# Optimization experiments

Measured on AMD Instinct MI355X. Metric: run time of the kernel, lower is better.

## Reference

```python
import jax, jax.numpy as jnp
import numpy as np

D = 1024           # input_size
D2 = 2 * D         # hidden width of the three inner linears
OUT = 1024         # output_size
S = 8192           # tokens per example


def setup_inputs() -> dict:
    key = jax.random.key(0)
    ks = jax.random.split(key, 11)
    def lin(k, fan_in, fan_out):
        bound = 1.0 / np.sqrt(fan_in)
        kw, kb = jax.random.split(k)
        W = jax.random.uniform(kw, (fan_in, fan_out), jnp.float32, -bound, bound)
        b = jax.random.uniform(kb, (fan_out,), jnp.float32, -bound, bound)
        return W, b
    W_in, b_in = lin(ks[0], D, D2)      # reading_example_input
    W_out, b_out = lin(ks[1], D, D2)    # reading_example_output
    W_cat, b_cat = lin(ks[2], D2, D2)   # concatenated_layer_map
    W_fin, b_fin = lin(ks[3], D2, OUT)  # final_map
    return {
        "input_embedding": jax.random.normal(ks[4], (1, S, D), jnp.float32),
        "output_embedding": jax.random.normal(ks[5], (1, S, D), jnp.float32),
        "random_augmentation": jax.random.normal(ks[6], (1, S, D), jnp.float32),
        "W_in": W_in, "b_in": b_in,
        "W_out": W_out, "b_out": b_out,
        "W_cat": W_cat, "b_cat": b_cat,
        "W_fin": W_fin, "b_fin": b_fin,
    }


def reference(input_embedding, output_embedding, random_augmentation,
              W_in, b_in, W_out, b_out, W_cat, b_cat, W_fin, b_fin):
    def march(x, y):
        # x, y: [1, S, D]
        iq = jax.nn.softmax(x @ W_in + b_in, axis=-1)[0]    # [S, 2D]
        oq = jax.nn.softmax(y @ W_out + b_out, axis=-1)[0]  # [S, 2D]
        cat = jnp.concatenate((x, y), axis=-1)[0]           # [S, 2D]
        icm = jax.nn.softmax(cat @ W_cat + b_cat, axis=-1)  # [S, 2D]
        iqk = iq.T @ icm                                    # [2D, 2D]
        oqk = oq.T @ icm                                    # [2D, 2D]
        meta = jax.nn.relu(iqk @ oqk.T)                     # [2D, 2D]
        scale = jnp.sqrt(jnp.float32(icm.shape[-1]))
        res = (icm @ meta) / scale                          # [S, 2D]
        return jax.nn.relu(res @ W_fin + b_fin)             # [S, OUT]

    transformation = march(input_embedding, output_embedding)
    random_desc = march(input_embedding, random_augmentation)
    return (transformation, random_desc)
```

## Files before the change

kernel.cpp:

```cpp
#include <hip/hip_runtime.h>

#define S_TOK 8192
#define DIM   1024
#define DIM2  2048
#define OUTN  1024

typedef __bf16 bf16x8 __attribute__((ext_vector_type(8)));
typedef float  f32x4  __attribute__((ext_vector_type(4)));
typedef short  s16x8  __attribute__((ext_vector_type(8)));
typedef unsigned short u16x4 __attribute__((ext_vector_type(4)));

__device__ __forceinline__ unsigned short f2bf(float x) {
  unsigned u = __builtin_bit_cast(unsigned, x);
  u = (u + 0x7FFFu + ((u >> 16) & 1u)) >> 16;
  return (unsigned short)u;
}
__device__ __forceinline__ float bf2f(unsigned short u) {
  return __builtin_bit_cast(float, (unsigned)u << 16);
}

__device__ __forceinline__ void gld_lds16(const void* g, void* l) {
  auto* g1 = reinterpret_cast<__attribute__((address_space(1))) unsigned*>(
      (unsigned long long)g);
  auto* l3 = reinterpret_cast<__attribute__((address_space(3))) unsigned*>(
      (unsigned long long)l);
  __builtin_amdgcn_global_load_lds(g1, l3, 16, 0, 0);
}

__device__ __forceinline__ int lds_off(int idx, int k) {
  int b = (idx << 7) + (k << 1);
  b ^= ((idx ^ (idx >> 3)) & 7) << 4;
  return b;
}

__global__ __launch_bounds__(256) void cvt_f32_bf16(const float* __restrict__ in,
                                                    unsigned short* __restrict__ out, int n4) {
  int i = blockIdx.x * 256 + threadIdx.x;
  if (i >= n4) return;
  float4 v = ((const float4*)in)[i];
  u16x4 o;
  o[0] = f2bf(v.x); o[1] = f2bf(v.y); o[2] = f2bf(v.z); o[3] = f2bf(v.w);
  *(u16x4*)(out + (size_t)i * 4) = o;
}

template <int F32IN>
__global__ __launch_bounds__(256) void transpose_to_bf16(const void* __restrict__ in,
                                                         unsigned short* __restrict__ out,
                                                         int R, int C) {
  __shared__ unsigned short t[64 * 64];
  const int r0 = blockIdx.y << 6, c0 = blockIdx.x << 6;
  const int tid = threadIdx.x;
#pragma unroll
  for (int i = 0; i < 2; ++i) {
    int ch = tid + (i << 8);
    int r = ch >> 3, c8 = (ch & 7) << 3;
    s16x8 w;
    if (F32IN) {
      const float* p = (const float*)in + (size_t)(r0 + r) * C + c0 + c8;
      float4 a = *(const float4*)p, b = *(const float4*)(p + 4);
      w[0] = (short)f2bf(a.x); w[1] = (short)f2bf(a.y);
      w[2] = (short)f2bf(a.z); w[3] = (short)f2bf(a.w);
      w[4] = (short)f2bf(b.x); w[5] = (short)f2bf(b.y);
      w[6] = (short)f2bf(b.z); w[7] = (short)f2bf(b.w);
    } else {
      w = *(const s16x8*)((const unsigned short*)in + (size_t)(r0 + r) * C + c0 + c8);
    }
    int sw = ((r ^ (r >> 3)) & 7) << 3;
    *(s16x8*)&t[(r << 6) + (c8 ^ sw)] = w;
  }
  __syncthreads();
#pragma unroll
  for (int i = 0; i < 2; ++i) {
    int ch = tid + (i << 8);
    int c = ch >> 3, r8 = (ch & 7) << 3;
    s16x8 w;
#pragma unroll
    for (int j = 0; j < 8; ++j) {
      int rr = r8 + j;
      w[j] = (short)t[(rr << 6) + (c ^ (((rr ^ (rr >> 3)) & 7) << 3))];
    }
    *(s16x8*)(out + (size_t)(c0 + c) * R + r0 + r8) = w;
  }
}

struct SmTab { unsigned short* T[6]; };
__global__ __launch_bounds__(512) void softmax_cols(SmTab tab) {
  unsigned short* T = tab.T[blockIdx.y];
  const int tid = threadIdx.x;
  const int colg = tid & 63, seg = tid >> 6;
  const size_t c = ((size_t)blockIdx.x << 6) + colg;
  float m = -1e30f, s = 0.f;
  for (int n = seg; n < DIM2; n += 8) {
    float v = bf2f(T[(size_t)n * S_TOK + c]);
    float mn = fmaxf(m, v);
    s = s * __expf(m - mn) + __expf(v - mn);
    m = mn;
  }
  __shared__ float redm[512], reds[512];
  redm[tid] = m; reds[tid] = s;
  __syncthreads();
  if (seg == 0) {
    float M = m, S = s;
#pragma unroll
    for (int k = 1; k < 8; ++k) {
      float mk = redm[colg + (k << 6)], sk = reds[colg + (k << 6)];
      float mn = fmaxf(M, mk);
      S = S * __expf(M - mn) + sk * __expf(mk - mn);
      M = mn;
    }
    redm[colg] = M; reds[colg] = 1.0f / S;
  }
  __syncthreads();
  m = redm[colg];
  const float inv = reds[colg];
  for (int n = seg; n < DIM2; n += 8) {
    size_t idx = (size_t)n * S_TOK + c;
    T[idx] = f2bf(__expf(bf2f(T[idx]) - m) * inv);
  }
}

struct GPtr {
  const unsigned short* A[3];
  const unsigned short* Arow2[3];
  const unsigned short* B[3];
  const unsigned short* Bk2[3];
  const float* bias[3];
  void* C[3];
};

template <int ASPLIT, int BSPLIT, int BIAS_ROW, int OUT_BF16>
__global__ __launch_bounds__(256, 3) void gemm_nt(GPtr p, int lda, int ldb, int ldc,
                                                  int K, float scale, int do_relu) {
  __shared__ __align__(16) char lds[32768];
  char* As = lds;
  char* Bs = lds + 16384;
  const int z = blockIdx.z;
  const int tid  = threadIdx.x;
  const int lane = tid & 63;
  const int wave = tid >> 6;
  const int wm = (wave >> 1) << 6;
  const int wn = (wave & 1) << 6;
  const int m0 = blockIdx.y << 7;
  const int n0 = blockIdx.x << 7;

  const unsigned short* Au = p.A[z];
  int mb = m0;
  if (ASPLIT && m0 >= 2048) { Au = p.Arow2[z]; mb = m0 - 2048; }
  const unsigned short* B  = p.B[z];
  const unsigned short* B2 = BSPLIT ? p.Bk2[z] : B;
  const float* bias = p.bias[z];
  void* Cv = p.C[z];

  int srow[4], sgk[4];
#pragma unroll
  for (int i = 0; i < 4; ++i) {
    int c = (wave << 8) + (i << 6) + lane;
    int row = c >> 3, kc = c & 7;
    srow[i] = row;
    sgk[i]  = (kc ^ ((row ^ (row >> 3)) & 7)) << 3;
  }

  f32x4 acc[4][4];
#pragma unroll
  for (int i = 0; i < 4; ++i)
#pragma unroll
    for (int j = 0; j < 4; ++j) acc[i][j] = {0.f, 0.f, 0.f, 0.f};

  for (int k0 = 0; k0 < K; k0 += 64) {
    const unsigned short* bsrc = B;
    int kb = k0;
    if (BSPLIT && k0 >= DIM) { bsrc = B2; kb = k0 - DIM; }
#pragma unroll
    for (int i = 0; i < 4; ++i) {
      char* dA = As + (((wave << 2) + i) << 10);
      char* dB = Bs + (((wave << 2) + i) << 10);
      gld_lds16(Au   + (size_t)(mb + srow[i]) * lda + k0 + sgk[i], dA);
      gld_lds16(bsrc + (size_t)(n0 + srow[i]) * ldb + kb + sgk[i], dB);
    }
    __syncthreads();
#pragma unroll
    for (int ks = 0; ks < 2; ++ks) {
      bf16x8 af[4], bfr[4];
      int kk = (ks << 5) + ((lane >> 4) << 3);
#pragma unroll
      for (int t = 0; t < 4; ++t) {
        af[t]  = *(const bf16x8*)(As + lds_off(wm + (t << 4) + (lane & 15), kk));
        bfr[t] = *(const bf16x8*)(Bs + lds_off(wn + (t << 4) + (lane & 15), kk));
      }
#pragma unroll
      for (int mt = 0; mt < 4; ++mt)
#pragma unroll
        for (int nt = 0; nt < 4; ++nt)
          acc[mt][nt] = __builtin_amdgcn_mfma_f32_16x16x32_bf16(af[mt], bfr[nt], acc[mt][nt], 0, 0, 0);
    }
    __syncthreads();
  }

#pragma unroll
  for (int nt = 0; nt < 4; ++nt) {
    int col = n0 + wn + (nt << 4) + (lane & 15);
    float bcol = (!BIAS_ROW && bias) ? bias[col] : 0.0f;
#pragma unroll
    for (int mt = 0; mt < 4; ++mt) {
      f32x4 a = acc[mt][nt];
#pragma unroll
      for (int r = 0; r < 4; ++r) {
        int rowg = m0 + wm + (mt << 4) + ((lane >> 4) << 2) + r;
        float bv = BIAS_ROW ? (bias ? bias[rowg] : 0.0f) : bcol;
        float v = a[r] * scale + bv;
        if (do_relu) v = fmaxf(v, 0.0f);
        if (OUT_BF16) ((unsigned short*)Cv)[(size_t)rowg * ldc + col] = f2bf(v);
        else          ((float*)Cv)[(size_t)rowg * ldc + col] = v;
      }
    }
  }
}

template <int ASPLIT, int BSPLIT, int BIAS_ROW, int OUT_BF16>
__global__ __launch_bounds__(512, 2) void gemm256(GPtr p, int lda, int ldb, int ldc,
                                                  int K, float scale, int do_relu) {
  __shared__ __align__(16) char lds[131072];
  const int z = blockIdx.z;
  const int tid  = threadIdx.x;
  const int lane = tid & 63;
  const int wave = tid >> 6;
  const int wm   = wave >> 2;
  const int wn   = wave & 3;

  const int gx = gridDim.x;
  const int nwg = gx * gridDim.y;
  int id = blockIdx.y * gx + blockIdx.x;
  id = (id & 7) * (nwg >> 3) + (id >> 3);
  const int n0 = (id % gx) << 8;
  const int m0 = (id / gx) << 8;

  const unsigned short* Au = p.A[z];
  int mb = m0;
  if (ASPLIT && m0 >= 2048) { Au = p.Arow2[z]; mb = m0 - 2048; }
  const unsigned short* Bp = p.B[z];
  const float* bias = p.bias[z];
  void* Cv = p.C[z];

  const int NT = K >> 6;

  int srow_[2], skel_[2];
#pragma unroll
  for (int i = 0; i < 2; ++i) {
    int row = (i << 7) + (wave << 4) + (lane >> 2);
    srow_[i] = row;
    skel_[i] = ((lane & 3) ^ ((row >> 1) & 3)) << 3;
  }
  const unsigned short* aB[2];
  const unsigned short* bB[2];
  const unsigned short* b2B[2];
#pragma unroll
  for (int i = 0; i < 2; ++i) {
    aB[i]  = Au + (size_t)(mb + srow_[i]) * lda + skel_[i];
    bB[i]  = Bp + (size_t)(n0 + srow_[i]) * ldb + skel_[i];
    b2B[i] = BSPLIT ? (p.Bk2[z] + (size_t)(n0 + srow_[i]) * ldb + skel_[i] - DIM)
                    : bB[i];
  }

  auto stage_unit = [&](int t, int u) {
    const int k0 = t << 6;
    const int h  = u >> 1;
    char* base = lds + ((t & 1) << 16) + ((u & 1) << 15) + (h << 14) + (wave << 10);
#pragma unroll
    for (int i = 0; i < 2; ++i) {
      const unsigned short* src;
      if (u & 1) src = ((BSPLIT && k0 >= DIM) ? b2B[i] : bB[i]) + k0 + (h << 5);
      else       src = aB[i] + k0 + (h << 5);
      gld_lds16(src, base + (i << 13));
    }
  };

  auto rdA = [&](const char* buf, int h, int mf) -> bf16x8 {
    int row = (wm << 7) + (mf << 4) + (lane & 15);
    int col = (lane >> 4) ^ ((row >> 1) & 3);
    return *(const bf16x8*)(buf + (h << 14) + (row << 6) + (col << 4));
  };
  auto rdB = [&](const char* buf, int h, int nf) -> bf16x8 {
    int row = (wn << 6) + (nf << 4) + (lane & 15);
    int col = (lane >> 4) ^ ((row >> 1) & 3);
    return *(const bf16x8*)(buf + 32768 + (h << 14) + (row << 6) + (col << 4));
  };

  f32x4 acc[8][4];
#pragma unroll
  for (int i = 0; i < 8; ++i)
#pragma unroll
    for (int j = 0; j < 4; ++j) acc[i][j] = {0.f, 0.f, 0.f, 0.f};

  stage_unit(0, 0); stage_unit(0, 1); stage_unit(0, 2); stage_unit(0, 3);

  for (int t = 0; t < NT; ++t) {
    const char* buf = lds + ((t & 1) << 16);
    const bool more = (t + 1 < NT);
    bf16x8 aq[4], bq[4];

    if (more) { stage_unit(t + 1, 0); asm volatile("s_waitcnt vmcnt(6)" ::: "memory"); }
    else      { asm volatile("s_waitcnt vmcnt(4)" ::: "memory"); }
    __builtin_amdgcn_s_barrier();
    __builtin_amdgcn_sched_barrier(0);
#pragma unroll
    for (int nf = 0; nf < 4; ++nf) bq[nf] = rdB(buf, 0, nf);
#pragma unroll
    for (int mf = 0; mf < 4; ++mf) aq[mf] = rdA(buf, 0, mf);
    __builtin_amdgcn_s_setprio(1);
#pragma unroll
    for (int mf = 0; mf < 4; ++mf)
#pragma unroll
      for (int nf = 0; nf < 4; ++nf)
        acc[mf][nf] = __builtin_amdgcn_mfma_f32_16x16x32_bf16(aq[mf], bq[nf], acc[mf][nf], 0, 0, 0);
    __builtin_amdgcn_s_setprio(0);
    __builtin_amdgcn_s_barrier();

#pragma unroll
    for (int mf = 0; mf < 4; ++mf) aq[mf] = rdA(buf, 0, mf + 4);
    if (more) stage_unit(t + 1, 1);
    __builtin_amdgcn_s_setprio(1);
#pragma unroll
    for (int mf = 0; mf < 4; ++mf)
#pragma unroll
      for (int nf = 0; nf < 4; ++nf)
        acc[mf + 4][nf] = __builtin_amdgcn_mfma_f32_16x16x32_bf16(aq[mf], bq[nf], acc[mf + 4][nf], 0, 0, 0);
    __builtin_amdgcn_s_setprio(0);
    __builtin_amdgcn_s_barrier();

    if (more) { stage_unit(t + 1, 2); asm volatile("s_waitcnt vmcnt(6)" ::: "memory"); }
    else      { asm volatile("s_waitcnt vmcnt(0)" ::: "memory"); }
    __builtin_amdgcn_s_barrier();
    __builtin_amdgcn_sched_barrier(0);
#pragma unroll
    for (int nf = 0; nf < 4; ++nf) bq[nf] = rdB(buf, 1, nf);
#pragma unroll
    for (int mf = 0; mf < 4; ++mf) aq[mf] = rdA(buf, 1, mf);
    __builtin_amdgcn_s_setprio(1);
#pragma unroll
    for (int mf = 0; mf < 4; ++mf)
#pragma unroll
      for (int nf = 0; nf < 4; ++nf)
        acc[mf][nf] = __builtin_amdgcn_mfma_f32_16x16x32_bf16(aq[mf], bq[nf], acc[mf][nf], 0, 0, 0);
    __builtin_amdgcn_s_setprio(0);
    __builtin_amdgcn_s_barrier();

#pragma unroll
    for (int mf = 0; mf < 4; ++mf) aq[mf] = rdA(buf, 1, mf + 4);
    if (more) stage_unit(t + 1, 3);
    __builtin_amdgcn_s_setprio(1);
#pragma unroll
    for (int mf = 0; mf < 4; ++mf)
#pragma unroll
      for (int nf = 0; nf < 4; ++nf)
        acc[mf + 4][nf] = __builtin_amdgcn_mfma_f32_16x16x32_bf16(aq[mf], bq[nf], acc[mf + 4][nf], 0, 0, 0);
    __builtin_amdgcn_s_setprio(0);
    __builtin_amdgcn_s_barrier();
  }

#pragma unroll
  for (int nf = 0; nf < 4; ++nf) {
    int col = n0 + (wn << 6) + (nf << 4) + (lane & 15);
    float bcol = (!BIAS_ROW && bias) ? bias[col] : 0.0f;
#pragma unroll
    for (int mf = 0; mf < 8; ++mf) {
      f32x4 a = acc[mf][nf];
#pragma unroll
      for (int r = 0; r < 4; ++r) {
        int rowg = m0 + (wm << 7) + (mf << 4) + ((lane >> 4) << 2) + r;
        float bv = BIAS_ROW ? (bias ? bias[rowg] : 0.0f) : bcol;
        float v = a[r] * scale + bv;
        if (do_relu) v = fmaxf(v, 0.0f);
        if (OUT_BF16) ((unsigned short*)Cv)[(size_t)rowg * ldc + col] = f2bf(v);
        else          ((float*)Cv)[(size_t)rowg * ldc + col] = v;
      }
    }
  }
}

extern "C" void kernel_launch(void* const* d_in, const int* in_sizes, int n_in,
                              void* d_out, int out_size, void* d_ws, size_t ws_size,
                              hipStream_t stream) {
  const float* X   = (const float*)d_in[0];
  const float* Y   = (const float*)d_in[1];
  const float* R   = (const float*)d_in[2];
  const float* Wi  = (const float*)d_in[3];
  const float* bi  = (const float*)d_in[4];
  const float* Wo  = (const float*)d_in[5];
  const float* bo  = (const float*)d_in[6];
  const float* Wc  = (const float*)d_in[7];
  const float* bc  = (const float*)d_in[8];
  const float* Wf  = (const float*)d_in[9];
  const float* bf_ = (const float*)d_in[10];
  float* out = (float*)d_out;

  char* ws = (char*)d_ws;
  size_t off = 0;
  auto alloc = [&](size_t b) { char* p = ws + off; off += (b + 255) & ~(size_t)255; return p; };
  unsigned short* Xb   = (unsigned short*)alloc((size_t)S_TOK * DIM  * 2);
  unsigned short* Yb   = (unsigned short*)alloc((size_t)S_TOK * DIM  * 2);
  unsigned short* Rb   = (unsigned short*)alloc((size_t)S_TOK * DIM  * 2);
  unsigned short* WiT  = (unsigned short*)alloc((size_t)DIM2 * DIM  * 2);
  unsigned short* WoT  = (unsigned short*)alloc((size_t)DIM2 * DIM  * 2);
  unsigned short* WcT  = (unsigned short*)alloc((size_t)DIM2 * DIM2 * 2);
  unsigned short* WfT  = (unsigned short*)alloc((size_t)OUTN * DIM2 * 2);
  unsigned short* iqT  = (unsigned short*)alloc((size_t)DIM2 * S_TOK * 2);
  unsigned short* oqT0 = (unsigned short*)alloc((size_t)DIM2 * S_TOK * 2);
  unsigned short* oqT1 = (unsigned short*)alloc((size_t)DIM2 * S_TOK * 2);
  unsigned short* icmT0= (unsigned short*)alloc((size_t)DIM2 * S_TOK * 2);
  unsigned short* icmT1= (unsigned short*)alloc((size_t)DIM2 * S_TOK * 2);
  unsigned short* iqk0 = Xb;
  unsigned short* oqk0 = Xb + (size_t)DIM2*DIM2;
  unsigned short* iqk1 = Yb;
  unsigned short* oqk1 = Yb + (size_t)DIM2*DIM2;
  unsigned short* meta0= iqT;
  unsigned short* meta1= iqT + (size_t)DIM2*DIM2;
  unsigned short* MWT0 = iqT + (size_t)2*DIM2*DIM2;
  unsigned short* MWT1 = iqT + (size_t)2*DIM2*DIM2 + (size_t)OUTN*DIM2;
  unsigned short* icm0 = oqT0;
  unsigned short* icm1 = oqT1;

  auto cvt = [&](const float* s, unsigned short* d, int n) {
    int n4 = n >> 2;
    cvt_f32_bf16<<<dim3((n4 + 255) / 256), dim3(256), 0, stream>>>(s, d, n4);
  };
  cvt(X, Xb, S_TOK * DIM);
  cvt(Y, Yb, S_TOK * DIM);
  cvt(R, Rb, S_TOK * DIM);
  transpose_to_bf16<1><<<dim3(DIM2 / 64, DIM  / 64), 256, 0, stream>>>(Wi, WiT, DIM,  DIM2);
  transpose_to_bf16<1><<<dim3(DIM2 / 64, DIM  / 64), 256, 0, stream>>>(Wo, WoT, DIM,  DIM2);
  transpose_to_bf16<1><<<dim3(DIM2 / 64, DIM2 / 64), 256, 0, stream>>>(Wc, WcT, DIM2, DIM2);
  transpose_to_bf16<1><<<dim3(OUTN / 64, DIM2 / 64), 256, 0, stream>>>(Wf, WfT, DIM2, OUTN);

  const float rscale = 0.022097086912079608f;

  {
    GPtr g{};
    g.A[0] = WiT; g.A[1] = WoT; g.A[2] = WoT;
    g.B[0] = Xb;  g.B[1] = Yb;  g.B[2] = Rb;
    g.bias[0] = bi; g.bias[1] = bo; g.bias[2] = bo;
    g.C[0] = iqT; g.C[1] = oqT0; g.C[2] = oqT1;
    gemm256<0,0,1,1><<<dim3(S_TOK/256, DIM2/256, 3), 512, 0, stream>>>(
        g, DIM, DIM, S_TOK, DIM, 1.f, 0);
  }
  {
    GPtr g{};
    g.A[0] = WcT; g.A[1] = WcT;
    g.B[0] = Xb;  g.B[1] = Xb;
    g.Bk2[0] = Yb; g.Bk2[1] = Rb;
    g.bias[0] = bc; g.bias[1] = bc;
    g.C[0] = icmT0; g.C[1] = icmT1;
    gemm256<0,1,1,1><<<dim3(S_TOK/256, DIM2/256, 2), 512, 0, stream>>>(
        g, DIM2, DIM, S_TOK, DIM2, 1.f, 0);
  }
  {
    SmTab st{};
    st.T[0] = iqT; st.T[1] = oqT0; st.T[2] = oqT1; st.T[3] = icmT0; st.T[4] = icmT1;
    softmax_cols<<<dim3(S_TOK / 64, 5), dim3(512), 0, stream>>>(st);
  }
  {
    GPtr g{};
    g.A[0] = iqT; g.A[1] = iqT;
    g.Arow2[0] = oqT0; g.Arow2[1] = oqT1;
    g.B[0] = icmT0; g.B[1] = icmT1;
    g.C[0] = iqk0; g.C[1] = iqk1;
    gemm256<1,0,0,1><<<dim3(DIM2/256, 4096/256, 2), 512, 0, stream>>>(
        g, S_TOK, S_TOK, DIM2, S_TOK, 1.f, 0);
  }
  transpose_to_bf16<0><<<dim3(S_TOK / 64, DIM2 / 64), 256, 0, stream>>>(icmT0, icm0, DIM2, S_TOK);
  transpose_to_bf16<0><<<dim3(S_TOK / 64, DIM2 / 64), 256, 0, stream>>>(icmT1, icm1, DIM2, S_TOK);
  {
    GPtr g{};
    g.A[0] = iqk0; g.A[1] = iqk1;
    g.B[0] = oqk0; g.B[1] = oqk1;
    g.C[0] = meta0; g.C[1] = meta1;
    gemm_nt<0,0,0,1><<<dim3(DIM2/128, DIM2/128, 2), 256, 0, stream>>>(
        g, DIM2, DIM2, DIM2, DIM2, 1.f, 1);
  }
  {
    GPtr g{};
    g.A[0] = WfT; g.A[1] = WfT;
    g.B[0] = meta0; g.B[1] = meta1;
    g.C[0] = MWT0; g.C[1] = MWT1;
    gemm_nt<0,0,0,1><<<dim3(DIM2/128, OUTN/128, 2), 256, 0, stream>>>(
        g, DIM2, DIM2, DIM2, DIM2, rscale, 0);
  }
  {
    GPtr g{};
    g.A[0] = icm0; g.A[1] = icm1;
    g.B[0] = MWT0; g.B[1] = MWT1;
    g.bias[0] = bf_; g.bias[1] = bf_;
    g.C[0] = out; g.C[1] = out + (size_t)S_TOK * OUTN;
    gemm256<0,0,0,0><<<dim3(OUTN/256, S_TOK/256, 2), 512, 0, stream>>>(
        g, DIM2, DIM2, OUTN, DIM2, 1.f, 1);
  }
  (void)in_sizes; (void)n_in; (void)out_size; (void)ws_size;
}
```

Before: 924.9 us.

## Batch small launches: merge converts, weight transposes, first GEMMs, fuse icm transpose

The three fp32-to-bf16 conversions become one launch, and the four weight transposes become another. The two first-stage GEMM launches (iq/oq and icm) are merged into a single 5-slice launch, with K and lda read per slice. The icm transposes are folded into the meta gemm_nt launch as extra z-slices, so they run concurrently with that GEMM. This cuts launch count and idle tails between kernels, at the cost of more argument-struct indirection. The second gemm_nt call has NZG=2 but grid z=2, so no transpose branch runs there.

```diff
diff --git a/kernel.cpp b/kernel.cpp
--- a/kernel.cpp
+++ b/kernel.cpp
@@ -33,40 +33,40 @@
   return b;
 }
 
-__global__ __launch_bounds__(256) void cvt_f32_bf16(const float* __restrict__ in,
-                                                    unsigned short* __restrict__ out, int n4) {
+struct CvtTab { const float* in[3]; unsigned short* out[3]; };
+__global__ __launch_bounds__(256) void cvt_f32_bf16_3(CvtTab t) {
+  const float* in = t.in[blockIdx.y];
+  unsigned short* out = t.out[blockIdx.y];
   int i = blockIdx.x * 256 + threadIdx.x;
-  if (i >= n4) return;
   float4 v = ((const float4*)in)[i];
   u16x4 o;
   o[0] = f2bf(v.x); o[1] = f2bf(v.y); o[2] = f2bf(v.z); o[3] = f2bf(v.w);
   *(u16x4*)(out + (size_t)i * 4) = o;
 }
 
-template <int F32IN>
-__global__ __launch_bounds__(256) void transpose_to_bf16(const void* __restrict__ in,
-                                                         unsigned short* __restrict__ out,
-                                                         int R, int C) {
-  __shared__ unsigned short t[64 * 64];
+struct WtTab { const float* in[4]; unsigned short* out[4]; int R[4]; int C[4]; };
+__global__ __launch_bounds__(256) void transpose_w4(WtTab t) {
+  const int z = blockIdx.z;
+  const int R = t.R[z], C = t.C[z];
   const int r0 = blockIdx.y << 6, c0 = blockIdx.x << 6;
+  if (r0 >= R || c0 >= C) return;
+  const float* in = t.in[z];
+  unsigned short* out = t.out[z];
+  __shared__ unsigned short tl[64 * 64];
   const int tid = threadIdx.x;
 #pragma unroll
   for (int i = 0; i < 2; ++i) {
     int ch = tid + (i << 8);
     int r = ch >> 3, c8 = (ch & 7) << 3;
+    const float* p = in + (size_t)(r0 + r) * C + c0 + c8;
+    float4 a = *(const float4*)p, b = *(const float4*)(p + 4);
     s16x8 w;
-    if (F32IN) {
-      const float* p = (const float*)in + (size_t)(r0 + r) * C + c0 + c8;
-      float4 a = *(const float4*)p, b = *(const float4*)(p + 4);
-      w[0] = (short)f2bf(a.x); w[1] = (short)f2bf(a.y);
-      w[2] = (short)f2bf(a.z); w[3] = (short)f2bf(a.w);
-      w[4] = (short)f2bf(b.x); w[5] = (short)f2bf(b.y);
-      w[6] = (short)f2bf(b.z); w[7] = (short)f2bf(b.w);
-    } else {
-      w = *(const s16x8*)((const unsigned short*)in + (size_t)(r0 + r) * C + c0 + c8);
-    }
+    w[0] = (short)f2bf(a.x); w[1] = (short)f2bf(a.y);
+    w[2] = (short)f2bf(a.z); w[3] = (short)f2bf(a.w);
+    w[4] = (short)f2bf(b.x); w[5] = (short)f2bf(b.y);
+    w[6] = (short)f2bf(b.z); w[7] = (short)f2bf(b.w);
     int sw = ((r ^ (r >> 3)) & 7) << 3;
-    *(s16x8*)&t[(r << 6) + (c8 ^ sw)] = w;
+    *(s16x8*)&tl[(r << 6) + (c8 ^ sw)] = w;
   }
   __syncthreads();
 #pragma unroll
@@ -77,7 +77,7 @@
 #pragma unroll
     for (int j = 0; j < 8; ++j) {
       int rr = r8 + j;
-      w[j] = (short)t[(rr << 6) + (c ^ (((rr ^ (rr >> 3)) & 7) << 3))];
+      w[j] = (short)tl[(rr << 6) + (c ^ (((rr ^ (rr >> 3)) & 7) << 3))];
     }
     *(s16x8*)(out + (size_t)(c0 + c) * R + r0 + r8) = w;
   }
@@ -120,34 +120,72 @@
 }
 
 struct GPtr {
-  const unsigned short* A[3];
-  const unsigned short* Arow2[3];
-  const unsigned short* B[3];
-  const unsigned short* Bk2[3];
-  const float* bias[3];
-  void* C[3];
+  const unsigned short* A[6];
+  const unsigned short* Arow2[6];
+  const unsigned short* B[6];
+  const unsigned short* Bk2[6];
+  const float* bias[6];
+  void* C[6];
+  int Ks[6];
+  int ldas[6];
 };
-
-template <int ASPLIT, int BSPLIT, int BIAS_ROW, int OUT_BF16>
-__global__ __launch_bounds__(256, 3) void gemm_nt(GPtr p, int lda, int ldb, int ldc,
-                                                  int K, float scale, int do_relu) {
+struct TPar { const unsigned short* src[2]; unsigned short* dst[2]; };
+
+template <int BIAS_ROW, int OUT_BF16, int NZG>
+__global__ __launch_bounds__(256, 3) void gemm_nt(GPtr p, TPar tp, int ldb, int ldc,
+                                                  float scale, int do_relu) {
   __shared__ __align__(16) char lds[32768];
+  const int z = blockIdx.z;
+  const int tid  = threadIdx.x;
+
+  if (NZG >= 0 && z >= NZG) {
+    const unsigned short* src = tp.src[z - NZG];
+    unsigned short* dst = tp.dst[z - NZG];
+    unsigned short* tl = (unsigned short*)lds;
+    const int nblk = gridDim.x * gridDim.y;
+    int bid = blockIdx.y * gridDim.x + blockIdx.x;
+    for (int it = bid; it < (DIM2 / 64) * (S_TOK / 64); it += nblk) {
+      int tx = it & (S_TOK / 64 - 1), ty = it >> 7;
+      int r0 = ty << 6, c0 = tx << 6;
+#pragma unroll
+      for (int i = 0; i < 2; ++i) {
+        int ch = tid + (i << 8);
+        int r = ch >> 3, c8 = (ch & 7) << 3;
+        s16x8 w = *(const s16x8*)(src + (size_t)(r0 + r) * S_TOK + c0 + c8);
+        int sw = ((r ^ (r >> 3)) & 7) << 3;
+        *(s16x8*)&tl[(r << 6) + (c8 ^ sw)] = w;
+      }
+      __syncthreads();
+#pragma unroll
+      for (int i = 0; i < 2; ++i) {
+        int ch = tid + (i << 8);
+        int c = ch >> 3, r8 = (ch & 7) << 3;
+        s16x8 w;
+#pragma unroll
+        for (int j = 0; j < 8; ++j) {
+          int rr = r8 + j;
+          w[j] = (short)tl[(rr << 6) + (c ^ (((rr ^ (rr >> 3)) & 7) << 3))];
+        }
+        *(s16x8*)(dst + (size_t)(c0 + c) * DIM2 + r0 + r8) = w;
+      }
+      __syncthreads();
+    }
+    return;
+  }
+
   char* As = lds;
   char* Bs = lds + 16384;
-  const int z = blockIdx.z;
-  const int tid  = threadIdx.x;
   const int lane = tid & 63;
   const int wave = tid >> 6;
   const int wm = (wave >> 1) << 6;
   const int wn = (wave & 1) << 6;
   const int m0 = blockIdx.y << 7;
   const int n0 = blockIdx.x << 7;
+  const int lda = p.ldas[z];
+  const int K = p.Ks[z];
 
   const unsigned short* Au = p.A[z];
-  int mb = m0;
-  if (ASPLIT && m0 >= 2048) { Au = p.Arow2[z]; mb = m0 - 2048; }
   const unsigned short* B  = p.B[z];
-  const unsigned short* B2 = BSPLIT ? p.Bk2[z] : B;
   const float* bias = p.bias[z];
   void* Cv = p.C[z];
 
@@ -167,15 +205,12 @@
     for (int j = 0; j < 4; ++j) acc[i][j] = {0.f, 0.f, 0.f, 0.f};
 
   for (int k0 = 0; k0 < K; k0 += 64) {
-    const unsigned short* bsrc = B;
-    int kb = k0;
-    if (BSPLIT && k0 >= DIM) { bsrc = B2; kb = k0 - DIM; }
 #pragma unroll
     for (int i = 0; i < 4; ++i) {
       char* dA = As + (((wave << 2) + i) << 10);
       char* dB = Bs + (((wave << 2) + i) << 10);
-      gld_lds16(Au   + (size_t)(mb + srow[i]) * lda + k0 + sgk[i], dA);
-      gld_lds16(bsrc + (size_t)(n0 + srow[i]) * ldb + kb + sgk[i], dB);
+      gld_lds16(Au + (size_t)(m0 + srow[i]) * lda + k0 + sgk[i], dA);
+      gld_lds16(B  + (size_t)(n0 + srow[i]) * ldb + k0 + sgk[i], dB);
     }
     __syncthreads();
 #pragma unroll
@@ -217,8 +252,8 @@
 }
 
 template <int ASPLIT, int BSPLIT, int BIAS_ROW, int OUT_BF16>
-__global__ __launch_bounds__(512, 2) void gemm256(GPtr p, int lda, int ldb, int ldc,
-                                                  int K, float scale, int do_relu) {
+__global__ __launch_bounds__(512, 2) void gemm256(GPtr p, int ldb, int ldc,
+                                                  float scale, int do_relu) {
   __shared__ __align__(16) char lds[131072];
   const int z = blockIdx.z;
   const int tid  = threadIdx.x;
@@ -226,6 +261,8 @@
   const int wave = tid >> 6;
   const int wm   = wave >> 2;
   const int wn   = wave & 3;
+  const int lda  = p.ldas[z];
+  const int K    = p.Ks[z];
 
   const int gx = gridDim.x;
   const int nwg = gx * gridDim.y;
@@ -419,38 +456,37 @@
   unsigned short* icm0 = oqT0;
   unsigned short* icm1 = oqT1;
 
-  auto cvt = [&](const float* s, unsigned short* d, int n) {
-    int n4 = n >> 2;
-    cvt_f32_bf16<<<dim3((n4 + 255) / 256), dim3(256), 0, stream>>>(s, d, n4);
-  };
-  cvt(X, Xb, S_TOK * DIM);
-  cvt(Y, Yb, S_TOK * DIM);
-  cvt(R, Rb, S_TOK * DIM);
-  transpose_to_bf16<1><<<dim3(DIM2 / 64, DIM  / 64), 256, 0, stream>>>(Wi, WiT, DIM,  DIM2);
-  transpose_to_bf16<1><<<dim3(DIM2 / 64, DIM  / 64), 256, 0, stream>>>(Wo, WoT, DIM,  DIM2);
-  transpose_to_bf16<1><<<dim3(DIM2 / 64, DIM2 / 64), 256, 0, stream>>>(Wc, WcT, DIM2, DIM2);
-  transpose_to_bf16<1><<<dim3(OUTN / 64, DIM2 / 64), 256, 0, stream>>>(Wf, WfT, DIM2, OUTN);
+  {
+    CvtTab t{};
+    t.in[0] = X; t.in[1] = Y; t.in[2] = R;
+    t.out[0] = Xb; t.out[1] = Yb; t.out[2] = Rb;
+    cvt_f32_bf16_3<<<dim3((S_TOK * DIM / 4) / 256, 3), 256, 0, stream>>>(t);
+  }
+  {
+    WtTab t{};
+    t.in[0] = Wi; t.out[0] = WiT; t.R[0] = DIM;  t.C[0] = DIM2;
+    t.in[1] = Wo; t.out[1] = WoT; t.R[1] = DIM;  t.C[1] = DIM2;
+    t.in[2] = Wc; t.out[2] = WcT; t.R[2] = DIM2; t.C[2] = DIM2;
+    t.in[3] = Wf; t.out[3] = WfT; t.R[3] = DIM2; t.C[3] = OUTN;
+    transpose_w4<<<dim3(32, 32, 4), 256, 0, stream>>>(t);
+  }
 
   const float rscale = 0.022097086912079608f;
 
   {
     GPtr g{};
-    g.A[0] = WiT; g.A[1] = WoT; g.A[2] = WoT;
-    g.B[0] = Xb;  g.B[1] = Yb;  g.B[2] = Rb;
-    g.bias[0] = bi; g.bias[1] = bo; g.bias[2] = bo;
-    g.C[0] = iqT; g.C[1] = oqT0; g.C[2] = oqT1;
-    gemm256<0,0,1,1><<<dim3(S_TOK/256, DIM2/256, 3), 512, 0, stream>>>(
-        g, DIM, DIM, S_TOK, DIM, 1.f, 0);
-  }
-  {
-    GPtr g{};
-    g.A[0] = WcT; g.A[1] = WcT;
-    g.B[0] = Xb;  g.B[1] = Xb;
-    g.Bk2[0] = Yb; g.Bk2[1] = Rb;
-    g.bias[0] = bc; g.bias[1] = bc;
-    g.C[0] = icmT0; g.C[1] = icmT1;
-    gemm256<0,1,1,1><<<dim3(S_TOK/256, DIM2/256, 2), 512, 0, stream>>>(
-        g, DIM2, DIM, S_TOK, DIM2, 1.f, 0);
+    g.A[0] = WiT; g.B[0] = Xb; g.Bk2[0] = Xb; g.bias[0] = bi; g.C[0] = iqT;
+    g.Ks[0] = DIM; g.ldas[0] = DIM;
+    g.A[1] = WoT; g.B[1] = Yb; g.Bk2[1] = Yb; g.bias[1] = bo; g.C[1] = oqT0;
+    g.Ks[1] = DIM; g.ldas[1] = DIM;
+    g.A[2] = WoT; g.B[2] = Rb; g.Bk2[2] = Rb; g.bias[2] = bo; g.C[2] = oqT1;
+    g.Ks[2] = DIM; g.ldas[2] = DIM;
+    g.A[3] = WcT; g.B[3] = Xb; g.Bk2[3] = Yb; g.bias[3] = bc; g.C[3] = icmT0;
+    g.Ks[3] = DIM2; g.ldas[3] = DIM2;
+    g.A[4] = WcT; g.B[4] = Xb; g.Bk2[4] = Rb; g.bias[4] = bc; g.C[4] = icmT1;
+    g.Ks[4] = DIM2; g.ldas[4] = DIM2;
+    gemm256<0,1,1,1><<<dim3(S_TOK/256, DIM2/256, 5), 512, 0, stream>>>(
+        g, DIM, S_TOK, 1.f, 0);
   }
   {
     SmTab st{};
@@ -463,35 +499,38 @@
     g.Arow2[0] = oqT0; g.Arow2[1] = oqT1;
     g.B[0] = icmT0; g.B[1] = icmT1;
     g.C[0] = iqk0; g.C[1] = iqk1;
+    g.Ks[0] = S_TOK; g.Ks[1] = S_TOK;
+    g.ldas[0] = S_TOK; g.ldas[1] = S_TOK;
     gemm256<1,0,0,1><<<dim3(DIM2/256, 4096/256, 2), 512, 0, stream>>>(
-        g, S_TOK, S_TOK, DIM2, S_TOK, 1.f, 0);
-  }
-  transpose_to_bf16<0><<<dim3(S_TOK / 64, DIM2 / 64), 256, 0, stream>>>(icmT0, icm0, DIM2, S_TOK);
-  transpose_to_bf16<0><<<dim3(S_TOK / 64, DIM2 / 64), 256, 0, stream>>>(icmT1, icm1, DIM2, S_TOK);
+        g, S_TOK, DIM2, 1.f, 0);
+  }
   {
     GPtr g{};
-    g.A[0] = iqk0; g.A[1] = iqk1;
-    g.B[0] = oqk0; g.B[1] = oqk1;
-    g.C[0] = meta0; g.C[1] = meta1;
-    gemm_nt<0,0,0,1><<<dim3(DIM2/128, DIM2/128, 2), 256, 0, stream>>>(
-        g, DIM2, DIM2, DIM2, DIM2, 1.f, 1);
+    g.A[0] = iqk0; g.B[0] = oqk0; g.C[0] = meta0; g.Ks[0] = DIM2; g.ldas[0] = DIM2;
+    g.A[1] = iqk1; g.B[1] = oqk1; g.C[1] = meta1; g.Ks[1] = DIM2; g.ldas[1] = DIM2;
+    TPar tp{};
+    tp.src[0] = icmT0; tp.dst[0] = icm0;
+    tp.src[1] = icmT1; tp.dst[1] = icm1;
+    gemm_nt<0,1,2><<<dim3(DIM2/128, DIM2/128, 4), 256, 0, stream>>>(
+        g, tp, DIM2, DIM2, 1.f, 1);
   }
   {
     GPtr g{};
-    g.A[0] = WfT; g.A[1] = WfT;
-    g.B[0] = meta0; g.B[1] = meta1;
-    g.C[0] = MWT0; g.C[1] = MWT1;
-    gemm_nt<0,0,0,1><<<dim3(DIM2/128, OUTN/128, 2), 256, 0, stream>>>(
-        g, DIM2, DIM2, DIM2, DIM2, rscale, 0);
+    g.A[0] = WfT; g.B[0] = meta0; g.C[0] = MWT0; g.Ks[0] = DIM2; g.ldas[0] = DIM2;
+    g.A[1] = WfT; g.B[1] = meta1; g.C[1] = MWT1; g.Ks[1] = DIM2; g.ldas[1] = DIM2;
+    TPar tp{};
+    gemm_nt<0,1,2><<<dim3(DIM2/128, OUTN/128, 2), 256, 0, stream>>>(
+        g, tp, DIM2, DIM2, rscale, 0);
   }
   {
     GPtr g{};
-    g.A[0] = icm0; g.A[1] = icm1;
-    g.B[0] = MWT0; g.B[1] = MWT1;
-    g.bias[0] = bf_; g.bias[1] = bf_;
-    g.C[0] = out; g.C[1] = out + (size_t)S_TOK * OUTN;
+    g.A[0] = icm0; g.B[0] = MWT0; g.bias[0] = bf_; g.C[0] = out;
+    g.Ks[0] = DIM2; g.ldas[0] = DIM2;
+    g.A[1] = icm1; g.B[1] = MWT1; g.bias[1] = bf_;
+    g.C[1] = out + (size_t)S_TOK * OUTN;
+    g.Ks[1] = DIM2; g.ldas[1] = DIM2;
     gemm256<0,0,0,0><<<dim3(OUTN/256, S_TOK/256, 2), 512, 0, stream>>>(
-        g, DIM2, DIM2, OUTN, DIM2, 1.f, 1);
+        g, DIM2, OUTN, 1.f, 1);
   }
   (void)in_sizes; (void)n_in; (void)out_size; (void)ws_size;
 }
```

After: 901.8 us. 1.03x faster.
